# Optimization experiments

Hardware: AMD Instinct MI355X
Metric: run time of the kernel (lower is better)

Reference implementation:

```python
import jax, jax.numpy as jnp
import numpy as np

K = 32          # kernel_size == per-unit image side
GRID = 128      # SOM grid side (units)
H = K * GRID    # full SOM canvas side = 4096
EPS = 1e-8      # variance-weighting stabilizer


def setup_inputs() -> dict:
    key = jax.random.key(0)
    k1, k2, k3 = jax.random.split(key, 3)
    input_image = jax.random.uniform(k1, (K, K), dtype=jnp.float32)
    som_matrix = jax.random.uniform(k2, (H, H), dtype=jnp.float32)
    # variances kept strictly positive
    som_running_variances = jax.random.uniform(k3, (H, H), dtype=jnp.float32) + 0.1
    return {
        "input_image": input_image,
        "som_matrix": som_matrix,
        "som_running_variances": som_running_variances,
    }


def _box_sum(x, k):
    """k x k stride-1 VALID box-sum via integral image (avoids O(N*k^2) patches)."""
    s = jnp.cumsum(jnp.cumsum(x, axis=0), axis=1)
    s = jnp.pad(s, ((1, 0), (1, 0)))  # [H+1, H+1]
    return s[k:, k:] - s[:-k, k:] - s[k:, :-k] + s[:-k, :-k]  # [H-k+1, H-k+1]


def reference(input_image, som_matrix, som_running_variances):
    # build(): kernel = tile(input_image, som_grid)
    kernel = jnp.tile(input_image, (H // K, H // K))  # [H, H]
    # util.global_variance_distance: variance-weighted squared distance per pixel
    dist = (kernel - som_matrix) ** 2 / (som_running_variances + EPS)  # [H, H]
    # stride-1 k x k patch extraction + per-patch sum == box filter
    return _box_sum(dist, K)  # [H-K+1, H-K+1]
```

## Files before the change

kernel.cpp:

```cpp
#include <hip/hip_runtime.h>
#include <hip/hip_bf16.h>

#define HH 4096
#define KK 32
#define OH 4065
#define NB 225
#define BC 256
#define RCHUNK 64
#define GR 8
#define NSUB (RCHUNK / GR)

__device__ __forceinline__ void barrier_lds_only() {
    asm volatile("" ::: "memory");
    __builtin_amdgcn_s_waitcnt(0xC07F);
    __builtin_amdgcn_s_barrier();
    asm volatile("" ::: "memory");
}

__global__ __launch_bounds__(BC, 4) void som_fused(
    const float* __restrict__ img,
    const float* __restrict__ som,
    const float* __restrict__ var,
    float* __restrict__ out)
{
    __shared__ float simg[KK * KK];
    __shared__ float ldsv[2][GR][BC];

    const int tid  = threadIdx.x;
    const int lane = tid & 63;
    const int wv   = tid >> 6;

    for (int i = tid; i < KK * KK; i += BC) simg[i] = img[i];
    __syncthreads();

    const int c0   = blockIdx.x * NB;
    const int col  = c0 + tid;
    const int colc = col < HH ? col : HH - 1;
    const int jc   = col & (KK - 1);
    const int r0   = blockIdx.y * RCHUNK;
    const int maxoff = HH - 1 - r0;

    const float* sp = som + (size_t)r0 * HH + colc;
    const float* vp = var + (size_t)r0 * HH + colc;

    float ring[KK];
    float sum = 0.f;
#pragma unroll
    for (int t = 0; t < KK; ++t) {
        const float s  = sp[t * HH];
        const float v  = vp[t * HH];
        const float im = simg[(t << 5) | jc];
        const float e  = im - s;
        const float d  = e * e * __builtin_amdgcn_rcpf(v + 1e-8f);
        ring[t] = d;
        sum += d;
    }

    float pf_s[2][GR], pf_v[2][GR];
#pragma unroll
    for (int k = 0; k < GR; ++k) {
        const int off = KK + k;
        pf_s[0][k] = sp[off * HH];
        pf_v[0][k] = vp[off * HH];
    }

#pragma unroll
    for (int sub = 0; sub < NSUB; ++sub) {
        const int buf = sub & 1;

#pragma unroll
        for (int k = 0; k < GR; ++k) {
            int off = KK + (sub + 1) * GR + k;
            off = off <= maxoff ? off : maxoff;
            pf_s[buf ^ 1][k] = sp[off * HH];
            pf_v[buf ^ 1][k] = vp[off * HH];
        }

#pragma unroll
        for (int k = 0; k < GR; ++k) {
            ldsv[buf][k][tid] = sum;
            const float s  = pf_s[buf][k];
            const float v  = pf_v[buf][k];
            const float im = simg[(((sub * GR + k) & (KK - 1)) << 5) | jc];
            const float e  = im - s;
            const float d  = e * e * __builtin_amdgcn_rcpf(v + 1e-8f);
            const int ri   = (sub * GR + k) & (KK - 1);
            sum += d - ring[ri];
            ring[ri] = d;
        }
        barrier_lds_only();

#pragma unroll
        for (int rr = 0; rr < 2; ++rr) {
            const int k = 2 * wv + rr;
            float4 x = *(const float4*)&ldsv[buf][k][lane * 4];
            const float p0 = x.x;
            const float p1 = p0 + x.y;
            const float p2 = p1 + x.z;
            const float p3 = p2 + x.w;
            float sc = p3;
#pragma unroll
            for (int off = 1; off < 64; off <<= 1) {
                const float t = __shfl_up(sc, off, 64);
                sc += (lane >= off) ? t : 0.f;
            }
            const float excl = sc - p3;
            float4 o;
            o.x = p0 + excl; o.y = p1 + excl; o.z = p2 + excl; o.w = p3 + excl;
            *(float4*)&ldsv[buf][k][lane * 4] = o;
        }
        barrier_lds_only();

        if (tid < NB && col < OH) {
#pragma unroll
            for (int k = 0; k < GR; ++k) {
                const int rout = r0 + sub * GR + k;
                if (rout < OH) {
                    const float hi = ldsv[buf][k][tid + KK - 1];
                    const float lo = (tid > 0) ? ldsv[buf][k][tid - 1] : 0.f;
                    out[(size_t)rout * OH + col] = hi - lo;
                }
            }
        }
    }
}

extern "C" void kernel_launch(void* const* d_in, const int* in_sizes, int n_in,
                              void* d_out, int out_size, void* d_ws, size_t ws_size,
                              hipStream_t stream) {
    (void)in_sizes; (void)n_in; (void)out_size; (void)d_ws; (void)ws_size;
    const float* img = (const float*)d_in[0];
    const float* som = (const float*)d_in[1];
    const float* var = (const float*)d_in[2];
    float* out = (float*)d_out;

    dim3 blk(BC);
    dim3 grd((OH + NB - 1) / NB,
             (OH + RCHUNK - 1) / RCHUNK);
    hipLaunchKernelGGL(som_fused, grd, blk, 0, stream, img, som, var, out);
}
```

Before: 200.2 us.

## Replace LDS prefix-scan blocks with single-wave kernels using shuffle horizontal sums

```diff
diff --git a/kernel.cpp b/kernel.cpp
--- a/kernel.cpp
+++ b/kernel.cpp
@@ -1,126 +1,123 @@
 #include <hip/hip_runtime.h>
-#include <hip/hip_bf16.h>
 
 #define HH 4096
 #define KK 32
 #define OH 4065
-#define NB 225
-#define BC 256
-#define RCHUNK 64
-#define GR 8
-#define NSUB (RCHUNK / GR)
+#define WPS 96
+#define NCOLS 128
+#define RCH 64
+#define PF 8
 
-__device__ __forceinline__ void barrier_lds_only() {
-    asm volatile("" ::: "memory");
-    __builtin_amdgcn_s_waitcnt(0xC07F);
-    __builtin_amdgcn_s_barrier();
-    asm volatile("" ::: "memory");
-}
-
-__global__ __launch_bounds__(BC, 4) void som_fused(
+__global__ __launch_bounds__(64) void som_wave(
     const float* __restrict__ img,
     const float* __restrict__ som,
     const float* __restrict__ var,
     float* __restrict__ out)
 {
     __shared__ float simg[KK * KK];
-    __shared__ float ldsv[2][GR][BC];
-
-    const int tid  = threadIdx.x;
-    const int lane = tid & 63;
-    const int wv   = tid >> 6;
-
-    for (int i = tid; i < KK * KK; i += BC) simg[i] = img[i];
+    const int l = threadIdx.x;
+    for (int i = l; i < KK * KK; i += 64) simg[i] = img[i];
     __syncthreads();
 
-    const int c0   = blockIdx.x * NB;
-    const int col  = c0 + tid;
-    const int colc = col < HH ? col : HH - 1;
-    const int jc   = col & (KK - 1);
-    const int r0   = blockIdx.y * RCHUNK;
-    const int maxoff = HH - 1 - r0;
+    const int slab  = blockIdx.x;
+    const int r0    = blockIdx.y * RCH;
+    const int cbase = slab * WPS;
+    const int c0    = cbase + 2 * l;
+    const int c0c   = c0 <= HH - 2 ? c0 : HH - 2;
+    const int jc0   = c0c & (KK - 1);
+    const bool maskE = (l <= 47) && (c0     <= OH - 1);
+    const bool maskO = (l <= 47) && (c0 + 1 <= OH - 1);
+    const int  rlimit = (r0 + RCH - 1 < OH - 1) ? r0 + RCH - 1 : OH - 1;
 
-    const float* sp = som + (size_t)r0 * HH + colc;
-    const float* vp = var + (size_t)r0 * HH + colc;
+    unsigned voff = (unsigned)(r0 * HH + c0c) * 4u;
+    const unsigned vmax  = (unsigned)((HH - 1) * HH + c0c) * 4u;
+    const unsigned vstep = HH * 4u;
+    unsigned vstore = (unsigned)(r0 * OH + c0) * 4u;
 
-    float ring[KK];
-    float sum = 0.f;
+    float2 pfs[PF], pfv[PF];
 #pragma unroll
-    for (int t = 0; t < KK; ++t) {
-        const float s  = sp[t * HH];
-        const float v  = vp[t * HH];
-        const float im = simg[(t << 5) | jc];
-        const float e  = im - s;
-        const float d  = e * e * __builtin_amdgcn_rcpf(v + 1e-8f);
-        ring[t] = d;
-        sum += d;
+    for (int p = 0; p < PF; ++p) {
+        pfs[p] = *(const float2*)((const char*)som + voff);
+        pfv[p] = *(const float2*)((const char*)var + voff);
+        voff = (voff + vstep <= vmax) ? voff + vstep : vmax;
     }
 
-    float pf_s[2][GR], pf_v[2][GR];
+    float ring0[KK], ring1[KK];
+    float sum0 = 0.f, sum1 = 0.f;
+
 #pragma unroll
-    for (int k = 0; k < GR; ++k) {
-        const int off = KK + k;
-        pf_s[0][k] = sp[off * HH];
-        pf_v[0][k] = vp[off * HH];
+    for (int k = 0; k < KK; ++k) {
+        const int slot = k & (PF - 1);
+        const float2 s2 = pfs[slot];
+        const float2 v2 = pfv[slot];
+        pfs[slot] = *(const float2*)((const char*)som + voff);
+        pfv[slot] = *(const float2*)((const char*)var + voff);
+        voff = (voff + vstep <= vmax) ? voff + vstep : vmax;
+
+        const float2 im = *(const float2*)&simg[(k << 5) | jc0];
+        const float e0 = im.x - s2.x;
+        const float d0 = e0 * e0 * __builtin_amdgcn_rcpf(v2.x + 1e-8f);
+        const float e1 = im.y - s2.y;
+        const float d1 = e1 * e1 * __builtin_amdgcn_rcpf(v2.y + 1e-8f);
+        const float V0 = sum0 + d0;
+        const float V1 = sum1 + d1;
+        if (k == KK - 1) {
+            float pr = V0 + V1;
+            pr += __shfl_down(pr, 1, 64);
+            pr += __shfl_down(pr, 2, 64);
+            pr += __shfl_down(pr, 4, 64);
+            pr += __shfl_down(pr, 8, 64);
+            const float ev = pr;
+            const float od = ev - V0 + __shfl_down(V0, 16, 64);
+            if (maskE) *(float*)((char*)out + vstore)     = ev;
+            if (maskO) *(float*)((char*)out + vstore + 4) = od;
+            vstore += OH * 4u;
+            sum0 = V0 - ring0[0];
+            sum1 = V1 - ring1[0];
+        } else {
+            sum0 = V0;
+            sum1 = V1;
+        }
+        ring0[k] = d0;
+        ring1[k] = d1;
     }
 
+#pragma unroll 1
+    for (int o = 1; o < 3; ++o) {
 #pragma unroll
-    for (int sub = 0; sub < NSUB; ++sub) {
-        const int buf = sub & 1;
+        for (int k = 0; k < KK; ++k) {
+            const int slot = k & (PF - 1);
+            const float2 s2 = pfs[slot];
+            const float2 v2 = pfv[slot];
+            pfs[slot] = *(const float2*)((const char*)som + voff);
+            pfv[slot] = *(const float2*)((const char*)var + voff);
+            voff = (voff + vstep <= vmax) ? voff + vstep : vmax;
 
-#pragma unroll
-        for (int k = 0; k < GR; ++k) {
-            int off = KK + (sub + 1) * GR + k;
-            off = off <= maxoff ? off : maxoff;
-            pf_s[buf ^ 1][k] = sp[off * HH];
-            pf_v[buf ^ 1][k] = vp[off * HH];
-        }
+            const float2 im = *(const float2*)&simg[(k << 5) | jc0];
+            const float e0 = im.x - s2.x;
+            const float d0 = e0 * e0 * __builtin_amdgcn_rcpf(v2.x + 1e-8f);
+            const float e1 = im.y - s2.y;
+            const float d1 = e1 * e1 * __builtin_amdgcn_rcpf(v2.y + 1e-8f);
+            const float V0 = sum0 + d0;
+            const float V1 = sum1 + d1;
 
-#pragma unroll
-        for (int k = 0; k < GR; ++k) {
-            ldsv[buf][k][tid] = sum;
-            const float s  = pf_s[buf][k];
-            const float v  = pf_v[buf][k];
-            const float im = simg[(((sub * GR + k) & (KK - 1)) << 5) | jc];
-            const float e  = im - s;
-            const float d  = e * e * __builtin_amdgcn_rcpf(v + 1e-8f);
-            const int ri   = (sub * GR + k) & (KK - 1);
-            sum += d - ring[ri];
-            ring[ri] = d;
-        }
-        barrier_lds_only();
-
-#pragma unroll
-        for (int rr = 0; rr < 2; ++rr) {
-            const int k = 2 * wv + rr;
-            float4 x = *(const float4*)&ldsv[buf][k][lane * 4];
-            const float p0 = x.x;
-            const float p1 = p0 + x.y;
-            const float p2 = p1 + x.z;
-            const float p3 = p2 + x.w;
-            float sc = p3;
-#pragma unroll
-            for (int off = 1; off < 64; off <<= 1) {
-                const float t = __shfl_up(sc, off, 64);
-                sc += (lane >= off) ? t : 0.f;
+            const int rout = r0 + o * KK + k - (KK - 1);
+            if (rout <= rlimit) {
+                float pr = V0 + V1;
+                pr += __shfl_down(pr, 1, 64);
+                pr += __shfl_down(pr, 2, 64);
+                pr += __shfl_down(pr, 4, 64);
+                pr += __shfl_down(pr, 8, 64);
+                const float ev = pr;
+                const float od = ev - V0 + __shfl_down(V0, 16, 64);
+                if (maskE) *(float*)((char*)out + vstore)     = ev;
+                if (maskO) *(float*)((char*)out + vstore + 4) = od;
             }
-            const float excl = sc - p3;
-            float4 o;
-            o.x = p0 + excl; o.y = p1 + excl; o.z = p2 + excl; o.w = p3 + excl;
-            *(float4*)&ldsv[buf][k][lane * 4] = o;
-        }
-        barrier_lds_only();
-
-        if (tid < NB && col < OH) {
-#pragma unroll
-            for (int k = 0; k < GR; ++k) {
-                const int rout = r0 + sub * GR + k;
-                if (rout < OH) {
-                    const float hi = ldsv[buf][k][tid + KK - 1];
-                    const float lo = (tid > 0) ? ldsv[buf][k][tid - 1] : 0.f;
-                    out[(size_t)rout * OH + col] = hi - lo;
-                }
-            }
+            vstore += OH * 4u;
+            sum0 = V0 - ring0[(k + 1) & (KK - 1)];
+            sum1 = V1 - ring1[(k + 1) & (KK - 1)];
+            ring0[k] = d0;
+            ring1[k] = d1;
         }
     }
 }
@@ -134,8 +131,8 @@
     const float* var = (const float*)d_in[2];
     float* out = (float*)d_out;
 
-    dim3 blk(BC);
-    dim3 grd((OH + NB - 1) / NB,
-             (OH + RCHUNK - 1) / RCHUNK);
-    hipLaunchKernelGGL(som_fused, grd, blk, 0, stream, img, som, var, out);
+    dim3 blk(64);
+    dim3 grd((OH + WPS - 1) / WPS,
+             (OH + RCH - 1) / RCH);
+    hipLaunchKernelGGL(som_wave, grd, blk, 0, stream, img, som, var, out);
 }
```

New measurement: 204.0 us. About the same (+1.9%).
